# Performance work log

Hardware: AMD Instinct MI355X
Metric: run time of the kernel (lower is better)

## Reference

```python
import jax, jax.numpy as jnp
import numpy as np

HIDDEN = 896
N_HEADS = 14
N_KV_HEADS = 2
HEAD_DIM = HIDDEN // N_HEADS  # 64
KV_GROUPS = N_HEADS // N_KV_HEADS  # 7
ROPE_THETA = 1000000.0


def rotate_half(x):
    x1, x2 = x[..., : x.shape[-1] // 2], x[..., x.shape[-1] // 2 :]
    return jnp.concatenate((-x2, x1), axis=-1)


def rope_tables(seq_len, dtype=jnp.float32):
    inv_freq = 1.0 / (ROPE_THETA ** (jnp.arange(0, HEAD_DIM, 2, dtype=jnp.float32) / HEAD_DIM))
    t = jnp.arange(seq_len, dtype=jnp.float32)
    freqs = jnp.outer(t, inv_freq)            # [S, D/2]
    emb = jnp.concatenate((freqs, freqs), -1)  # [S, D]
    return jnp.cos(emb).astype(dtype), jnp.sin(emb).astype(dtype)


def setup_inputs() -> dict:
    key = jax.random.key(0)
    ks = jax.random.split(key, 8)
    B, S = 2, 2048
    s = 0.02
    return {
        "hidden_states": jax.random.normal(ks[0], (B, S, HIDDEN), jnp.float32),
        "wq": jax.random.normal(ks[1], (HIDDEN, N_HEADS * HEAD_DIM), jnp.float32) * s,
        "bq": jnp.zeros((N_HEADS * HEAD_DIM,), jnp.float32),
        "wk": jax.random.normal(ks[2], (HIDDEN, N_KV_HEADS * HEAD_DIM), jnp.float32) * s,
        "bk": jnp.zeros((N_KV_HEADS * HEAD_DIM,), jnp.float32),
        "wv": jax.random.normal(ks[3], (HIDDEN, N_KV_HEADS * HEAD_DIM), jnp.float32) * s,
        "bv": jnp.zeros((N_KV_HEADS * HEAD_DIM,), jnp.float32),
        "wo": jax.random.normal(ks[4], (N_HEADS * HEAD_DIM, HIDDEN), jnp.float32) * s,
    }


def reference(hidden_states, wq, bq, wk, bk, wv, bv, wo):
    B, S, _ = hidden_states.shape
    q = (hidden_states @ wq + bq).reshape(B, S, N_HEADS, HEAD_DIM)
    k = (hidden_states @ wk + bk).reshape(B, S, N_KV_HEADS, HEAD_DIM)
    v = (hidden_states @ wv + bv).reshape(B, S, N_KV_HEADS, HEAD_DIM)

    cos, sin = rope_tables(S, hidden_states.dtype)
    cos, sin = cos[None, :, None, :], sin[None, :, None, :]
    q = q * cos + rotate_half(q) * sin
    k = k * cos + rotate_half(k) * sin

    # GQA broadcast: repeat kv heads to match query heads
    k = jnp.repeat(k, KV_GROUPS, axis=2)
    v = jnp.repeat(v, KV_GROUPS, axis=2)

    # [B, H, S, S]
    scores = jnp.einsum("bqhd,bkhd->bhqk", q, k) / jnp.sqrt(jnp.asarray(HEAD_DIM, hidden_states.dtype))
    mask = jnp.tril(jnp.ones((S, S), dtype=jnp.bool_))
    scores = jnp.where(mask[None, None, :, :], scores, jnp.asarray(-1e9, scores.dtype))
    attn = jax.nn.softmax(scores, axis=-1)
    out = jnp.einsum("bhqk,bkhd->bqhd", attn, v).reshape(B, S, N_HEADS * HEAD_DIM)
    return out @ wo
```

## Files before the change

kernel.cpp:

```cpp
#include <hip/hip_runtime.h>

#define HID 896
#define NQ 896
#define NKV 128
#define NQKV 1152
#define NH 14
#define NKVH 2
#define GQ 7
#define DH 64
#define SEQ 2048
#define BATCH 2
#define TOK (BATCH*SEQ)

typedef __attribute__((ext_vector_type(8))) short short8;
typedef __attribute__((ext_vector_type(4))) float f32x4;
typedef __attribute__((ext_vector_type(4))) unsigned short us4;

__device__ __forceinline__ unsigned short f2bf(float x) {
  unsigned int u = __builtin_bit_cast(unsigned int, x);
  u = (u + 0x7fffu + ((u >> 16) & 1u)) >> 16;
  return (unsigned short)u;
}
__device__ __forceinline__ float bf2f(unsigned short b) {
  return __builtin_bit_cast(float, (unsigned int)b << 16);
}
__device__ __forceinline__ f32x4 fzero4() {
  f32x4 z; z[0]=0.f; z[1]=0.f; z[2]=0.f; z[3]=0.f; return z;
}
__device__ __forceinline__ unsigned int cvt_pk_bf16(float lo, float hi) {
  unsigned int r;
  asm("v_cvt_pk_bf16_f32 %0, %1, %2" : "=v"(r) : "v"(lo), "v"(hi));
  return r;
}
__device__ __forceinline__ void gload_lds16(const unsigned short* g, unsigned short* l) {
  __builtin_amdgcn_global_load_lds(
      (const __attribute__((address_space(1))) void*)(const void*)g,
      (__attribute__((address_space(3))) void*)(void*)l, 16, 0, 0);
}

#define CVT_BLKS 3584
#define TRN_BLKS 448
#define BIAS_BLKS 5
#define TAB_BLKS 256
#define PREP_BLKS (CVT_BLKS + TRN_BLKS + BIAS_BLKS + TAB_BLKS)

__global__ void k_prep(const float* __restrict__ hs,
                       const float* __restrict__ wq, const float* __restrict__ bq,
                       const float* __restrict__ wk, const float* __restrict__ bk,
                       const float* __restrict__ wv, const float* __restrict__ bv,
                       const float* __restrict__ wo,
                       unsigned short* __restrict__ hb,
                       unsigned short* __restrict__ wqkvt,
                       unsigned short* __restrict__ wot,
                       float* __restrict__ bqkv,
                       float2* __restrict__ cs) {
  __shared__ unsigned short Ls[64*65];
  int blk = blockIdx.x, tid = threadIdx.x;
  if (blk < CVT_BLKS) {
    int i = blk*256 + tid;
    float4 v = ((const float4*)hs)[i];
    us4 o; o[0]=f2bf(v.x); o[1]=f2bf(v.y); o[2]=f2bf(v.z); o[3]=f2bf(v.w);
    ((us4*)hb)[i] = o;
    return;
  }
  blk -= CVT_BLKS;
  if (blk < TRN_BLKS) {
    const float* W; unsigned short* out; int K, N, n0, k0;
    if (blk < 196)      { W=wq; out=wqkvt;                        K=HID; N=NQ;  int t=blk;     n0=(t%14)*64; k0=(t/14)*64; }
    else if (blk < 224) { W=wk; out=wqkvt + (size_t)NQ*HID;       K=HID; N=NKV; int t=blk-196; n0=(t%2)*64;  k0=(t/2)*64; }
    else if (blk < 252) { W=wv; out=wqkvt + (size_t)(NQ+NKV)*HID; K=HID; N=NKV; int t=blk-224; n0=(t%2)*64;  k0=(t/2)*64; }
    else                { W=wo; out=wot;                          K=NQ;  N=HID; int t=blk-252; n0=(t%14)*64; k0=(t/14)*64; }
    #pragma unroll
    for (int i = 0; i < 16; ++i) {
      int idx = i*256 + tid;
      int r = idx >> 6, c = idx & 63;
      Ls[c*65 + r] = f2bf(W[(size_t)(k0 + r)*N + n0 + c]);
    }
    __syncthreads();
    #pragma unroll
    for (int i = 0; i < 16; ++i) {
      int idx = i*256 + tid;
      int r2 = idx >> 6, c2 = idx & 63;
      out[(size_t)(n0 + r2)*K + k0 + c2] = Ls[r2*65 + c2];
    }
    return;
  }
  blk -= TRN_BLKS;
  if (blk < BIAS_BLKS) {
    int i = blk*256 + tid;
    if (i < NQKV) {
      if (i < NQ) bqkv[i] = bq[i];
      else if (i < NQ + NKV) bqkv[i] = bk[i - NQ];
      else bqkv[i] = bv[i - NQ - NKV];
    }
    return;
  }
  blk -= BIAS_BLKS;
  {
    int i = blk*256 + tid;
    int s = i >> 5, dp = i & 31;
    float inv = __expf(-(float)(2*dp) * (13.815510557964274f / 64.0f));
    float f = (float)s * inv;
    cs[i] = make_float2(cosf(f), sinf(f));
  }
}

template<int OUTMODE>
__global__ __launch_bounds__(256, 4) void k_gemm_bt(
    const unsigned short* __restrict__ A,
    const unsigned short* __restrict__ Bt,
    const float* __restrict__ bias,
    const float2* __restrict__ cs,
    void* __restrict__ Cout,
    unsigned short* __restrict__ Qr,
    unsigned short* __restrict__ Kr,
    unsigned short* __restrict__ Vt,
    int M, int N, int K) {
  __shared__ unsigned short As[64*64];
  __shared__ unsigned short Bs[128*64];
  int tid = threadIdx.x;
  int lane = tid & 63, w = tid >> 6;
  int wr = w >> 1, wc = w & 1;
  int l15 = lane & 15, l4 = lane >> 4;
  int m0 = blockIdx.y * 64, n0 = blockIdx.x * 128;

  f32x4 acc[2][4];
  #pragma unroll
  for (int i = 0; i < 2; ++i)
    #pragma unroll
    for (int j = 0; j < 4; ++j) acc[i][j] = fzero4();

  int nkt = K >> 6;
  for (int kt = 0; kt < nkt; ++kt) {
    int k0 = kt << 6;
    #pragma unroll
    for (int t = 0; t < 2; ++t) {
      int chunk = t*256 + w*64 + lane;
      int row = chunk >> 3, sp = chunk & 7;
      int sl = sp ^ (row & 7);
      gload_lds16(A + (size_t)(m0+row)*K + k0 + sl*8, &As[(t*256 + w*64)*8]);
    }
    #pragma unroll
    for (int t = 0; t < 4; ++t) {
      int chunk = t*256 + w*64 + lane;
      int row = chunk >> 3, sp = chunk & 7;
      int sl = sp ^ (row & 7);
      gload_lds16(Bt + (size_t)(n0+row)*K + k0 + sl*8, &Bs[(t*256 + w*64)*8]);
    }
    __syncthreads();
    #pragma unroll
    for (int s = 0; s < 2; ++s) {
      short8 af[2], bfr[4];
      #pragma unroll
      for (int mi = 0; mi < 2; ++mi) {
        int row = wr*32 + mi*16 + l15;
        int slot = (s*4 + l4) ^ (row & 7);
        af[mi] = *reinterpret_cast<const short8*>(&As[row*64 + slot*8]);
      }
      #pragma unroll
      for (int ni = 0; ni < 4; ++ni) {
        int row = wc*64 + ni*16 + l15;
        int slot = (s*4 + l4) ^ (row & 7);
        bfr[ni] = *reinterpret_cast<const short8*>(&Bs[row*64 + slot*8]);
      }
      #pragma unroll
      for (int mi = 0; mi < 2; ++mi)
        #pragma unroll
        for (int ni = 0; ni < 4; ++ni)
          acc[mi][ni] = __builtin_amdgcn_mfma_f32_16x16x32_bf16(af[mi], bfr[ni], acc[mi][ni], 0, 0, 0);
    }
    __syncthreads();
  }

  if (OUTMODE == 1) {
    #pragma unroll
    for (int mi = 0; mi < 2; ++mi)
      #pragma unroll
      for (int ni = 0; ni < 4; ++ni)
        #pragma unroll
        for (int r = 0; r < 4; ++r) {
          int row = m0 + wr*32 + mi*16 + l4*4 + r;
          int col = n0 + wc*64 + ni*16 + l15;
          ((float*)Cout)[(size_t)row*N + col] = acc[mi][ni][r];
        }
    return;
  }

  int col0 = n0 + wc*64;
  #pragma unroll
  for (int mi = 0; mi < 2; ++mi) {
    #pragma unroll
    for (int r = 0; r < 4; ++r) {
      int row = m0 + wr*32 + mi*16 + l4*4 + r;
      int b = row >> 11, s = row & 2047;
      #pragma unroll
      for (int ni = 0; ni < 2; ++ni) {
        int dp = ni*16 + l15;
        float x1 = acc[mi][ni][r]   + bias[col0 + dp];
        float x2 = acc[mi][ni+2][r] + bias[col0 + dp + 32];
        if (col0 < NQ) {
          int h = col0 >> 6;
          float2 c2 = cs[s*32 + dp];
          size_t base = ((size_t)(b*NH + h)*SEQ + s)*64;
          Qr[base + dp]      = f2bf((x1*c2.x - x2*c2.y) * 0.125f);
          Qr[base + dp + 32] = f2bf((x2*c2.x + x1*c2.y) * 0.125f);
        } else if (col0 < NQ + NKV) {
          int kvh = (col0 - NQ) >> 6;
          float2 c2 = cs[s*32 + dp];
          size_t base = ((size_t)(b*NKVH + kvh)*SEQ + s)*64;
          Kr[base + dp]      = f2bf(x1*c2.x - x2*c2.y);
          Kr[base + dp + 32] = f2bf(x2*c2.x + x1*c2.y);
        } else {
          int kvh = (col0 - 1024) >> 6;
          size_t base = (size_t)(b*NKVH + kvh)*64;
          Vt[(base + dp)*SEQ + s]      = f2bf(x1);
          Vt[(base + dp + 32)*SEQ + s] = f2bf(x2);
        }
      }
    }
  }
}

__global__ __launch_bounds__(512, 2) void k_attn(
    const unsigned short* __restrict__ Q,
    const unsigned short* __restrict__ Kr,
    const unsigned short* __restrict__ Vt,
    unsigned short* __restrict__ Aout) {
  __shared__ __align__(16) unsigned short Kst[2][2][64*64];
  __shared__ __align__(16) unsigned short Vst[2][2][64*64];
  __shared__ __align__(16) unsigned short P_lds[8][16*64];
  int lane = threadIdx.x & 63, w = threadIdx.x >> 6;
  int grp = w >> 2, wsub = w & 3;
  int l15 = lane & 15, l4 = lane >> 4;
  int i = blockIdx.x, h = blockIdx.y, b = blockIdx.z;
  int qtH = 31 - i, qtL = i;
  int qt = grp ? qtL : qtH;
  int kvh = h / GQ;
  const unsigned short* Kb = Kr + ((size_t)(b*NKVH + kvh))*SEQ*64;
  const unsigned short* Vb = Vt + ((size_t)(b*NKVH + kvh))*64*SEQ;
  char* Pw = (char*)&P_lds[w][0];

  auto stage = [&](int slab, int bsel) {
    #pragma unroll
    for (int t = 0; t < 2; ++t) {
      int ks = slab*2 + t; if (ks > 31) ks = 31;
      int chunk = w*64 + lane;
      int row = chunk >> 3;
      int sl = (chunk & 7) ^ (row & 7);
      gload_lds16(Kb + (size_t)(ks*64 + row)*64 + sl*8, &Kst[bsel][t][chunk*8]);
      gload_lds16(Vb + (size_t)row*SEQ + ks*64 + sl*8, &Vst[bsel][t][chunk*8]);
    }
  };

  const unsigned short* Qb = Q + (((size_t)(b*NH + h))*SEQ + qt*64 + wsub*16) * 64;
  short8 qa[2];
  #pragma unroll
  for (int s = 0; s < 2; ++s)
    qa[s] = *reinterpret_cast<const short8*>(Qb + l15*64 + s*32 + l4*8);

  f32x4 acc[4];
  #pragma unroll
  for (int n = 0; n < 4; ++n) acc[n] = fzero4();
  float m_run = -__builtin_inff(), l_run = 0.0f;

  stage(0, 0);
  __syncthreads();
  int cur = 0;
  int nkt = qtH + 1;
  int nslab = (nkt + 1) >> 1;

  for (int s = 0; s < nslab; ++s) {
    if (s + 1 < nslab) stage(s + 1, cur ^ 1);
    #pragma unroll
    for (int t = 0; t < 2; ++t) {
      int ks = s*2 + t;
      if (ks <= qt) {
        const unsigned short* Ks = &Kst[cur][t][0];
        const unsigned short* Vs = &Vst[cur][t][0];
        f32x4 sa[4];
        #pragma unroll
        for (int n = 0; n < 4; ++n) sa[n] = fzero4();
        __builtin_amdgcn_s_setprio(1);
        #pragma unroll
        for (int si = 0; si < 2; ++si) {
          short8 kb[4];
          #pragma unroll
          for (int n = 0; n < 4; ++n) {
            int row = n*16 + l15;
            int slot = (si*4 + l4) ^ (row & 7);
            kb[n] = *reinterpret_cast<const short8*>(&Ks[row*64 + slot*8]);
          }
          #pragma unroll
          for (int n = 0; n < 4; ++n)
            sa[n] = __builtin_amdgcn_mfma_f32_16x16x32_bf16(kb[n], qa[si], sa[n], 0, 0, 0);
        }
        __builtin_amdgcn_s_setprio(0);
        if (ks == qt) {
          int q_glob = qt*64 + wsub*16 + l15;
          #pragma unroll
          for (int n = 0; n < 4; ++n)
            #pragma unroll
            for (int r = 0; r < 4; ++r) {
              int kpos = ks*64 + n*16 + l4*4 + r;
              if (kpos > q_glob) sa[n][r] = -1e30f;
            }
        }
        float t0 = fmaxf(fmaxf(sa[0][0],sa[0][1]), fmaxf(sa[0][2],sa[0][3]));
        float t1 = fmaxf(fmaxf(sa[1][0],sa[1][1]), fmaxf(sa[1][2],sa[1][3]));
        float t2 = fmaxf(fmaxf(sa[2][0],sa[2][1]), fmaxf(sa[2][2],sa[2][3]));
        float t3 = fmaxf(fmaxf(sa[3][0],sa[3][1]), fmaxf(sa[3][2],sa[3][3]));
        float tmax = fmaxf(fmaxf(t0,t1), fmaxf(t2,t3));
        tmax = fmaxf(tmax, __shfl_xor(tmax, 16));
        tmax = fmaxf(tmax, __shfl_xor(tmax, 32));
        float mn = fmaxf(m_run, tmax);
        float sc = __expf(m_run - mn);
        #pragma unroll
        for (int n = 0; n < 4; ++n)
          #pragma unroll
          for (int r = 0; r < 4; ++r) sa[n][r] = __expf(sa[n][r] - mn);
        float s0 = (sa[0][0]+sa[0][1]) + (sa[0][2]+sa[0][3]);
        float s1 = (sa[1][0]+sa[1][1]) + (sa[1][2]+sa[1][3]);
        float s2 = (sa[2][0]+sa[2][1]) + (sa[2][2]+sa[2][3]);
        float s3 = (sa[3][0]+sa[3][1]) + (sa[3][2]+sa[3][3]);
        float sum = (s0+s1) + (s2+s3);
        sum += __shfl_xor(sum, 16);
        sum += __shfl_xor(sum, 32);
        m_run = mn;
        l_run = l_run*sc + sum;
        #pragma unroll
        for (int n = 0; n < 4; ++n) acc[n] *= sc;
        #pragma unroll
        for (int n = 0; n < 4; ++n) {
          uint2 pk;
          pk.x = cvt_pk_bf16(sa[n][0], sa[n][1]);
          pk.y = cvt_pk_bf16(sa[n][2], sa[n][3]);
          int colbyte = n*32 + l4*8;
          int addr = l15*128 + ((((colbyte>>4) ^ (l15&7))) << 4) + (colbyte & 15);
          *reinterpret_cast<uint2*>(Pw + addr) = pk;
        }
        __builtin_amdgcn_s_setprio(1);
        #pragma unroll
        for (int s2i = 0; s2i < 2; ++s2i) {
          int pslot = (s2i*4 + l4) ^ (l15 & 7);
          short8 pa = *reinterpret_cast<const short8*>(Pw + l15*128 + pslot*16);
          #pragma unroll
          for (int n = 0; n < 4; ++n) {
            int row = n*16 + l15;
            int vslot = (s2i*4 + l4) ^ (row & 7);
            short8 vb = *reinterpret_cast<const short8*>(&Vs[row*64 + vslot*8]);
            acc[n] = __builtin_amdgcn_mfma_f32_16x16x32_bf16(vb, pa, acc[n], 0, 0, 0);
          }
        }
        __builtin_amdgcn_s_setprio(0);
      }
    }
    __syncthreads();
    cur ^= 1;
  }

  float inv = 1.0f / l_run;
  #pragma unroll
  for (int n = 0; n < 4; ++n) {
    uint2 pk;
    pk.x = cvt_pk_bf16(acc[n][0]*inv, acc[n][1]*inv);
    pk.y = cvt_pk_bf16(acc[n][2]*inv, acc[n][3]*inv);
    int colbyte = n*32 + l4*8;
    int addr = l15*128 + ((((colbyte>>4) ^ (l15&7))) << 4) + (colbyte & 15);
    *reinterpret_cast<uint2*>(Pw + addr) = pk;
  }
  int row = lane >> 2;
  int cb0 = (lane & 3) * 32;
  #pragma unroll
  for (int it = 0; it < 2; ++it) {
    int cb = cb0 + it*16;
    int slot = (cb >> 4) ^ (row & 7);
    short8 v = *reinterpret_cast<const short8*>(Pw + row*128 + slot*16);
    size_t tok = (size_t)b*SEQ + qt*64 + wsub*16 + row;
    *reinterpret_cast<short8*>(&Aout[tok*NQ + h*64 + (cb>>1)]) = v;
  }
}

extern "C" void kernel_launch(void* const* d_in, const int* in_sizes, int n_in,
                              void* d_out, int out_size, void* d_ws, size_t ws_size,
                              hipStream_t stream) {
  const float* hs = (const float*)d_in[0];
  const float* wq = (const float*)d_in[1];
  const float* bq = (const float*)d_in[2];
  const float* wk = (const float*)d_in[3];
  const float* bk = (const float*)d_in[4];
  const float* wv = (const float*)d_in[5];
  const float* bv = (const float*)d_in[6];
  const float* wo = (const float*)d_in[7];
  float* out = (float*)d_out;

  char* p = (char*)d_ws;
  auto alloc = [&](size_t bytes) { char* r = p; p += (bytes + 255) & ~(size_t)255; return r; };
  unsigned short* hb    = (unsigned short*)alloc((size_t)TOK*HID*2);
  unsigned short* wqkvt = (unsigned short*)alloc((size_t)NQKV*HID*2);
  unsigned short* wot   = (unsigned short*)alloc((size_t)HID*NQ*2);
  float*          bqkv  = (float*)alloc(NQKV*4);
  float2*         cs    = (float2*)alloc((size_t)SEQ*32*8);
  unsigned short* q_r   = (unsigned short*)alloc((size_t)BATCH*NH*SEQ*DH*2);
  unsigned short* k_r   = (unsigned short*)alloc((size_t)BATCH*NKVH*SEQ*DH*2);
  unsigned short* v_t   = (unsigned short*)alloc((size_t)BATCH*NKVH*DH*SEQ*2);
  unsigned short* attn  = (unsigned short*)alloc((size_t)TOK*NQ*2);

  k_prep<<<PREP_BLKS, 256, 0, stream>>>(hs, wq, bq, wk, bk, wv, bv, wo,
                                        hb, wqkvt, wot, bqkv, cs);
  k_gemm_bt<0><<<dim3(NQKV/128, TOK/64), 256, 0, stream>>>(
      hb, wqkvt, bqkv, cs, nullptr, q_r, k_r, v_t, TOK, NQKV, HID);
  k_attn<<<dim3(16, NH, BATCH), 512, 0, stream>>>(q_r, k_r, v_t, attn);
  k_gemm_bt<1><<<dim3(NQ/128, TOK/64), 256, 0, stream>>>(
      attn, wot, nullptr, nullptr, out, nullptr, nullptr, nullptr, TOK, NQ, HID);
}
```

Before: 91.43 us.

## Double-buffer GEMM LDS tiles, stage V transpose via LDS, defer softmax row-sum reduction

The projection GEMM now double-buffers its A/B LDS tiles so the next K-tile's global-to-LDS loads are issued before computing on the current one. Occupancy is lowered to 3 blocks per CU to fit the larger shared memory. The V output path now writes bias-added bf16 values into an LDS scratch area and then stores coalesced 16-byte rows into the transposed Vt layout, instead of doing scattered 2-byte stores. In attention, the cross-lane sum reduction of the softmax denominator moves out of the inner loop and runs once at the end. This relies on the per-lane partial sums being rescaled consistently.

```diff
diff --git a/kernel.cpp b/kernel.cpp
--- a/kernel.cpp
+++ b/kernel.cpp
@@ -106,7 +106,7 @@
 }
 
 template<int OUTMODE>
-__global__ __launch_bounds__(256, 4) void k_gemm_bt(
+__global__ __launch_bounds__(256, 3) void k_gemm_bt(
     const unsigned short* __restrict__ A,
     const unsigned short* __restrict__ Bt,
     const float* __restrict__ bias,
@@ -116,8 +116,8 @@
     unsigned short* __restrict__ Kr,
     unsigned short* __restrict__ Vt,
     int M, int N, int K) {
-  __shared__ unsigned short As[64*64];
-  __shared__ unsigned short Bs[128*64];
+  __shared__ unsigned short As[2][64*64];
+  __shared__ unsigned short Bs[2][128*64];
   int tid = threadIdx.x;
   int lane = tid & 63, w = tid >> 6;
   int wr = w >> 1, wc = w & 1;
@@ -130,24 +130,30 @@
     #pragma unroll
     for (int j = 0; j < 4; ++j) acc[i][j] = fzero4();
 
-  int nkt = K >> 6;
-  for (int kt = 0; kt < nkt; ++kt) {
+  auto stage = [&](int kt, int bsel) {
     int k0 = kt << 6;
     #pragma unroll
     for (int t = 0; t < 2; ++t) {
       int chunk = t*256 + w*64 + lane;
       int row = chunk >> 3, sp = chunk & 7;
       int sl = sp ^ (row & 7);
-      gload_lds16(A + (size_t)(m0+row)*K + k0 + sl*8, &As[(t*256 + w*64)*8]);
+      gload_lds16(A + (size_t)(m0+row)*K + k0 + sl*8, &As[bsel][(t*256 + w*64)*8]);
     }
     #pragma unroll
     for (int t = 0; t < 4; ++t) {
       int chunk = t*256 + w*64 + lane;
       int row = chunk >> 3, sp = chunk & 7;
       int sl = sp ^ (row & 7);
-      gload_lds16(Bt + (size_t)(n0+row)*K + k0 + sl*8, &Bs[(t*256 + w*64)*8]);
-    }
-    __syncthreads();
+      gload_lds16(Bt + (size_t)(n0+row)*K + k0 + sl*8, &Bs[bsel][(t*256 + w*64)*8]);
+    }
+  };
+
+  int nkt = K >> 6;
+  stage(0, 0);
+  __syncthreads();
+  int cur = 0;
+  for (int kt = 0; kt < nkt; ++kt) {
+    if (kt + 1 < nkt) stage(kt + 1, cur ^ 1);
     #pragma unroll
     for (int s = 0; s < 2; ++s) {
       short8 af[2], bfr[4];
@@ -155,13 +161,13 @@
       for (int mi = 0; mi < 2; ++mi) {
         int row = wr*32 + mi*16 + l15;
         int slot = (s*4 + l4) ^ (row & 7);
-        af[mi] = *reinterpret_cast<const short8*>(&As[row*64 + slot*8]);
+        af[mi] = *reinterpret_cast<const short8*>(&As[cur][row*64 + slot*8]);
       }
       #pragma unroll
       for (int ni = 0; ni < 4; ++ni) {
         int row = wc*64 + ni*16 + l15;
         int slot = (s*4 + l4) ^ (row & 7);
-        bfr[ni] = *reinterpret_cast<const short8*>(&Bs[row*64 + slot*8]);
+        bfr[ni] = *reinterpret_cast<const short8*>(&Bs[cur][row*64 + slot*8]);
       }
       #pragma unroll
       for (int mi = 0; mi < 2; ++mi)
@@ -170,6 +176,7 @@
           acc[mi][ni] = __builtin_amdgcn_mfma_f32_16x16x32_bf16(af[mi], bfr[ni], acc[mi][ni], 0, 0, 0);
     }
     __syncthreads();
+    cur ^= 1;
   }
 
   if (OUTMODE == 1) {
@@ -187,36 +194,62 @@
   }
 
   int col0 = n0 + wc*64;
-  #pragma unroll
-  for (int mi = 0; mi < 2; ++mi) {
-    #pragma unroll
-    for (int r = 0; r < 4; ++r) {
-      int row = m0 + wr*32 + mi*16 + l4*4 + r;
-      int b = row >> 11, s = row & 2047;
+  if (col0 < NQ + NKV) {
+    #pragma unroll
+    for (int mi = 0; mi < 2; ++mi) {
+      #pragma unroll
+      for (int r = 0; r < 4; ++r) {
+        int row = m0 + wr*32 + mi*16 + l4*4 + r;
+        int b = row >> 11, s = row & 2047;
+        #pragma unroll
+        for (int ni = 0; ni < 2; ++ni) {
+          int dp = ni*16 + l15;
+          float x1 = acc[mi][ni][r]   + bias[col0 + dp];
+          float x2 = acc[mi][ni+2][r] + bias[col0 + dp + 32];
+          float2 c2 = cs[s*32 + dp];
+          if (col0 < NQ) {
+            int h = col0 >> 6;
+            size_t base = ((size_t)(b*NH + h)*SEQ + s)*64;
+            Qr[base + dp]      = f2bf((x1*c2.x - x2*c2.y) * 0.125f);
+            Qr[base + dp + 32] = f2bf((x2*c2.x + x1*c2.y) * 0.125f);
+          } else {
+            int kvh = (col0 - NQ) >> 6;
+            size_t base = ((size_t)(b*NKVH + kvh)*SEQ + s)*64;
+            Kr[base + dp]      = f2bf(x1*c2.x - x2*c2.y);
+            Kr[base + dp + 32] = f2bf(x2*c2.x + x1*c2.y);
+          }
+        }
+      }
+    }
+  } else {
+    int kvh = (col0 - 1024) >> 6;
+    unsigned short* scr = &Bs[0][0] + w * (64*40);
+    #pragma unroll
+    for (int mi = 0; mi < 2; ++mi) {
       #pragma unroll
       for (int ni = 0; ni < 2; ++ni) {
-        int dp = ni*16 + l15;
-        float x1 = acc[mi][ni][r]   + bias[col0 + dp];
-        float x2 = acc[mi][ni+2][r] + bias[col0 + dp + 32];
-        if (col0 < NQ) {
-          int h = col0 >> 6;
-          float2 c2 = cs[s*32 + dp];
-          size_t base = ((size_t)(b*NH + h)*SEQ + s)*64;
-          Qr[base + dp]      = f2bf((x1*c2.x - x2*c2.y) * 0.125f);
-          Qr[base + dp + 32] = f2bf((x2*c2.x + x1*c2.y) * 0.125f);
-        } else if (col0 < NQ + NKV) {
-          int kvh = (col0 - NQ) >> 6;
-          float2 c2 = cs[s*32 + dp];
-          size_t base = ((size_t)(b*NKVH + kvh)*SEQ + s)*64;
-          Kr[base + dp]      = f2bf(x1*c2.x - x2*c2.y);
-          Kr[base + dp + 32] = f2bf(x2*c2.x + x1*c2.y);
-        } else {
-          int kvh = (col0 - 1024) >> 6;
-          size_t base = (size_t)(b*NKVH + kvh)*64;
-          Vt[(base + dp)*SEQ + s]      = f2bf(x1);
-          Vt[(base + dp + 32)*SEQ + s] = f2bf(x2);
+        #pragma unroll
+        for (int h2 = 0; h2 < 2; ++h2) {
+          int dp = ni*16 + l15 + h2*32;
+          float b0 = bias[col0 + dp];
+          f32x4 a = acc[mi][ni + h2*2];
+          uint2 pk;
+          pk.x = cvt_pk_bf16(a[0] + b0, a[1] + b0);
+          pk.y = cvt_pk_bf16(a[2] + b0, a[3] + b0);
+          *reinterpret_cast<uint2*>(&scr[dp*40 + mi*16 + l4*4]) = pk;
         }
       }
+    }
+    __syncthreads();
+    int srow0 = m0 + wr*32;
+    int b = srow0 >> 11, s0 = srow0 & 2047;
+    size_t vbase = (size_t)(b*NKVH + kvh)*64;
+    #pragma unroll
+    for (int p2 = 0; p2 < 4; ++p2) {
+      int dp = p2*16 + (lane >> 2);
+      int tok0 = (lane & 3) * 8;
+      short8 v = *reinterpret_cast<const short8*>(&scr[dp*40 + tok0]);
+      *reinterpret_cast<short8*>(&Vt[(vbase + dp)*SEQ + s0 + tok0]) = v;
     }
   }
 }
@@ -323,8 +356,6 @@
         float s2 = (sa[2][0]+sa[2][1]) + (sa[2][2]+sa[2][3]);
         float s3 = (sa[3][0]+sa[3][1]) + (sa[3][2]+sa[3][3]);
         float sum = (s0+s1) + (s2+s3);
-        sum += __shfl_xor(sum, 16);
-        sum += __shfl_xor(sum, 32);
         m_run = mn;
         l_run = l_run*sc + sum;
         #pragma unroll
@@ -358,7 +389,10 @@
     cur ^= 1;
   }
 
-  float inv = 1.0f / l_run;
+  float lt = l_run;
+  lt += __shfl_xor(lt, 16);
+  lt += __shfl_xor(lt, 32);
+  float inv = 1.0f / lt;
   #pragma unroll
   for (int n = 0; n < 4; ++n) {
     uint2 pk;
```

After: 87.97 us. 3.8% less time.
